# Kernel optimization log

Hardware: AMD Instinct MI355X
Metric: run time of the kernel (lower is better)

## Reference

```python
import jax, jax.numpy as jnp
import numpy as np
import math

B, N, D = 8, 2048, 1024
DK = D // 4
TOP_K = 32
SCALE = math.sqrt(DK)
NEG = -1000000000.0


def setup_inputs() -> dict:
    key = jax.random.key(0)
    k1, k2, k3, k4, k5 = jax.random.split(key, 5)
    lim = 1.0 / math.sqrt(D)
    return {
        "action_states": jax.random.normal(k1, (B, N, D), dtype=jnp.float32),
        "Wq": jax.random.uniform(k2, (D, DK), minval=-lim, maxval=lim, dtype=jnp.float32),
        "bq": jax.random.uniform(k3, (DK,), minval=-lim, maxval=lim, dtype=jnp.float32),
        "Wk": jax.random.uniform(k4, (D, DK), minval=-lim, maxval=lim, dtype=jnp.float32),
        "bk": jax.random.uniform(k5, (DK,), minval=-lim, maxval=lim, dtype=jnp.float32),
    }


def reference(action_states, Wq, bq, Wk, bk):
    # Q, K projections: (B, N, DK)
    Q = jnp.einsum("bnd,dk->bnk", action_states, Wq) + bq
    K = jnp.einsum("bnd,dk->bnk", action_states, Wk) + bk
    # scaled dot-product scores: (B, N, N)
    scores = jnp.einsum("bqk,bmk->bqm", Q, K) / SCALE
    # top-k sparsify per row + scatter mask
    topk_vals, topk_idx = jax.lax.top_k(scores, TOP_K)  # (B, N, K)
    bi = jnp.arange(B)[:, None, None]
    ni = jnp.arange(N)[None, :, None]
    mask = jnp.zeros_like(scores).at[bi, ni, topk_idx].set(1.0)
    scores = scores * mask + (1.0 - mask) * NEG
    return jax.nn.softmax(scores, axis=-1)
```

## Files before the change

### kernel.cpp

```cpp
#include <hip/hip_runtime.h>
#include <cstdint>
#include <cstddef>

#define B_   8
#define N_   2048
#define D_   1024
#define DK_  256
#define M_   (B_ * N_)
#define TOPK 32
#define NDIG 5

typedef unsigned short ushort_t;
typedef float  fvec4 __attribute__((ext_vector_type(4)));
typedef short  bvec8 __attribute__((ext_vector_type(8)));
typedef float  avec4 __attribute__((ext_vector_type(4)));
typedef int    ivec4 __attribute__((ext_vector_type(4)));

__device__ inline ushort_t f32_to_bf16_rn(float f) {
  unsigned u = __float_as_uint(f);
  u += 0x7fffu + ((u >> 16) & 1u);
  return (ushort_t)(u >> 16);
}
__device__ inline float bf16_to_f32(ushort_t u) {
  return __uint_as_float(((unsigned)u) << 16);
}


__global__ __launch_bounds__(256) void split_x_kernel(
    const float* __restrict__ X, signed char* __restrict__ Xdig)
{
  const size_t MK = (size_t)M_ * D_;
  const int total = (int)(MK / 4);
  for (int idx = blockIdx.x * 256 + threadIdx.x; idx < total;
       idx += gridDim.x * 256) {
    const fvec4 x = ((const fvec4*)X)[idx];
    unsigned pack[NDIG] = {0u, 0u, 0u, 0u, 0u};
#pragma unroll
    for (int e = 0; e < 4; e++) {
      float s = x[e] * 0.0625f * 128.f;
#pragma unroll
      for (int d = 0; d < NDIG; d++) {
        const float a = rintf(s);
        s = (s - a) * 128.f;
        pack[d] |= ((unsigned)((int)a & 0xff)) << (e * 8);
      }
    }
#pragma unroll
    for (int d = 0; d < NDIG; d++)
      ((unsigned*)(Xdig + (size_t)d * MK))[idx] = pack[d];
  }
}

__global__ __launch_bounds__(256) void split_w_kernel(
    const float* __restrict__ Wq, const float* __restrict__ Wk,
    signed char* __restrict__ Wdig)
{
  const size_t WK = (size_t)512 * 1024;
  const int cc = blockIdx.x;
  const float* Wp = (cc < 256) ? Wq : Wk;
  const int c = cc & 255;
  const int k0 = threadIdx.x * 4;
  unsigned pack[NDIG] = {0u, 0u, 0u, 0u, 0u};
#pragma unroll
  for (int e = 0; e < 4; e++) {
    float s = Wp[(size_t)(k0 + e) * DK_ + c] * 16.f * 128.f;
#pragma unroll
    for (int d = 0; d < NDIG; d++) {
      const float a = rintf(s);
      s = (s - a) * 128.f;
      pack[d] |= ((unsigned)((int)a & 0xff)) << (e * 8);
    }
  }
#pragma unroll
  for (int d = 0; d < NDIG; d++)
    ((unsigned*)(Wdig + (size_t)d * WK + (size_t)cc * 1024))[threadIdx.x] = pack[d];
}

__global__ __launch_bounds__(512) void ozaki_gemm_kernel(
    const signed char* __restrict__ Xdig, const signed char* __restrict__ Wdig,
    const float* __restrict__ bq, const float* __restrict__ bk,
    double* __restrict__ Qd, double* __restrict__ Kd,
    ushort_t* __restrict__ Qbf, ushort_t* __restrict__ Kbf)
{
  __shared__ __align__(16) char L[61440];
  const int tid  = threadIdx.x;
  const int lane = tid & 63;
  const int w    = tid >> 6;
  const int wm   = (w >> 2) * 32;
  const int wc   = (w & 3) * 32;
  const int m0   = blockIdx.y * 64;
  const int c0   = blockIdx.x * 128;
  const size_t MK = (size_t)M_ * D_;
  const size_t WK = (size_t)512 * 1024;

  ivec4 acc[NDIG][2][2];
#pragma unroll
  for (int s = 0; s < NDIG; s++)
#pragma unroll
    for (int mi = 0; mi < 2; mi++)
#pragma unroll
      for (int nj = 0; nj < 2; nj++) acc[s][mi][nj] = (ivec4)(0);

  for (int k0 = 0; k0 < D_; k0 += 64) {
    for (int c = tid; c < 1280; c += 512) {
      const int d = c >> 8, rem = c & 255, r = rem >> 2, kp = rem & 3;
      const ivec4 raw = *(const ivec4*)(Xdig + (size_t)d * MK +
                         (size_t)(m0 + r) * D_ + k0 + kp * 16);
      *(ivec4*)&L[d * 4096 + r * 64 + ((kp ^ (r & 3)) << 4)] = raw;
    }
    for (int c = tid; c < 2560; c += 512) {
      const int d = c >> 9, rem = c & 511, r = rem >> 2, kp = rem & 3;
      const ivec4 raw = *(const ivec4*)(Wdig + (size_t)d * WK +
                         (size_t)(c0 + r) * 1024 + k0 + kp * 16);
      *(ivec4*)&L[20480 + d * 8192 + r * 64 + ((kp ^ (r & 3)) << 4)] = raw;
    }
    __syncthreads();

    ivec4 afr[2][NDIG];
#pragma unroll
    for (int mi = 0; mi < 2; mi++) {
      const int r = wm + mi * 16 + (lane & 15);
      const int sl = (((lane >> 4) ^ (r & 3)) << 4);
#pragma unroll
      for (int d = 0; d < NDIG; d++)
        afr[mi][d] = *(const ivec4*)&L[d * 4096 + r * 64 + sl];
    }
#pragma unroll
    for (int nj = 0; nj < 2; nj++) {
      const int rc = wc + nj * 16 + (lane & 15);
      const int sl = (((lane >> 4) ^ (rc & 3)) << 4);
#pragma unroll
      for (int jd = 0; jd < NDIG; jd++) {
        const ivec4 bfr = *(const ivec4*)&L[20480 + jd * 8192 + rc * 64 + sl];
#pragma unroll
        for (int id = 0; id + jd < NDIG; id++)
#pragma unroll
          for (int mi = 0; mi < 2; mi++)
            acc[id + jd][mi][nj] = __builtin_amdgcn_mfma_i32_16x16x64_i8(
                afr[mi][id], bfr, acc[id + jd][mi][nj], 0, 0, 0);
      }
    }
    __syncthreads();
  }

  const double SCL[NDIG] = {0x1p-14, 0x1p-21, 0x1p-28, 0x1p-35, 0x1p-42};
#pragma unroll
  for (int nj = 0; nj < 2; nj++) {
    const int c = c0 + wc + nj * 16 + (lane & 15);
    const bool isQ = (c < 256);
    const int cw = isQ ? c : (c - 256);
    const double bias = (double)(isQ ? bq[cw] : bk[cw]);
#pragma unroll
    for (int mi = 0; mi < 2; mi++) {
#pragma unroll
      for (int ri = 0; ri < 4; ri++) {
        const int m = m0 + wm + mi * 16 + (lane >> 4) * 4 + ri;
        double val = bias;
#pragma unroll
        for (int s = 0; s < NDIG; s++)
          val += (double)acc[s][mi][nj][ri] * SCL[s];
        const size_t off = (size_t)m * DK_ + cw;
        if (isQ) { Qd[off] = val; Qbf[off] = f32_to_bf16_rn((float)val); }
        else     { Kd[off] = val; Kbf[off] = f32_to_bf16_rn((float)val); }
      }
    }
  }
}

__global__ __launch_bounds__(256) void proj_kernel(
    const float* __restrict__ X, const float* __restrict__ Wq,
    const float* __restrict__ bq, const float* __restrict__ Wk,
    const float* __restrict__ bk, double* __restrict__ Qd,
    double* __restrict__ Kd, ushort_t* __restrict__ Qbf,
    ushort_t* __restrict__ Kbf)
{
  __shared__ float As[16][132];
  __shared__ float Bs[16][132];
  const int tid = threadIdx.x;
  const int tx = tid & 15;
  const int ty = tid >> 4;
  const int m0 = blockIdx.y * 128;
  const int j0 = blockIdx.x * 128;
  const bool isQ = (j0 < 256);
  const float* Wp = isQ ? Wq : Wk;
  const float* bp = isQ ? bq : bk;
  const int jw = isQ ? j0 : (j0 - 256);

  double acc[8][8];
#pragma unroll
  for (int i = 0; i < 8; i++)
#pragma unroll
    for (int j = 0; j < 8; j++) acc[i][j] = 0.0;

  for (int k0 = 0; k0 < D_; k0 += 16) {
    {
      const int r = tid >> 2, k4 = (tid & 3) * 4;
#pragma unroll
      for (int p = 0; p < 2; p++) {
        const int m = r + 64 * p;
        const fvec4 v = *(const fvec4*)&X[(size_t)(m0 + m) * D_ + k0 + k4];
#pragma unroll
        for (int c = 0; c < 4; c++) As[k4 + c][m] = v[c];
      }
    }
    {
      const int k = tid >> 4, j8 = (tid & 15) * 8;
      const fvec4 v0 = *(const fvec4*)&Wp[(size_t)(k0 + k) * DK_ + jw + j8];
      const fvec4 v1 = *(const fvec4*)&Wp[(size_t)(k0 + k) * DK_ + jw + j8 + 4];
      *(fvec4*)&Bs[k][j8]     = v0;
      *(fvec4*)&Bs[k][j8 + 4] = v1;
    }
    __syncthreads();
#pragma unroll
    for (int kk = 0; kk < 16; kk++) {
      const fvec4 a0 = *(const fvec4*)&As[kk][ty * 8];
      const fvec4 a1 = *(const fvec4*)&As[kk][ty * 8 + 4];
      const fvec4 b0 = *(const fvec4*)&Bs[kk][tx * 8];
      const fvec4 b1 = *(const fvec4*)&Bs[kk][tx * 8 + 4];
      double a[8], b[8];
#pragma unroll
      for (int i = 0; i < 4; i++) {
        a[i] = (double)a0[i]; a[i + 4] = (double)a1[i];
        b[i] = (double)b0[i]; b[i + 4] = (double)b1[i];
      }
#pragma unroll
      for (int i = 0; i < 8; i++)
#pragma unroll
        for (int j = 0; j < 8; j++)
          acc[i][j] = fma(a[i], b[j], acc[i][j]);
    }
    __syncthreads();
  }

#pragma unroll
  for (int i = 0; i < 8; i++) {
    const int m = m0 + ty * 8 + i;
#pragma unroll
    for (int j = 0; j < 8; j++) {
      const int c = jw + tx * 8 + j;
      const double v = acc[i][j] + (double)bp[c];
      const size_t off = (size_t)m * DK_ + c;
      if (isQ) { Qd[off] = v; if (Qbf) Qbf[off] = f32_to_bf16_rn((float)v); }
      else     { Kd[off] = v; if (Kbf) Kbf[off] = f32_to_bf16_rn((float)v); }
    }
  }
}

__global__ __launch_bounds__(256) void score_bf16_kernel(
    const ushort_t* __restrict__ Qb, const ushort_t* __restrict__ Kb,
    float* __restrict__ outf, ushort_t* __restrict__ outbf)
{
  __shared__ ushort_t Asl[128 * 40];
  __shared__ ushort_t Bsl[128 * 40];
  const int tid = threadIdx.x;
  const int b  = blockIdx.z;
  const int q0 = blockIdx.y * 128;
  const int m0 = blockIdx.x * 128;
  const int w = tid >> 6, lane = tid & 63;
  const int wq = (w >> 1) * 64, wm = (w & 1) * 64;
  const int rsel = lane & 15, ksel = (lane >> 4) * 8;

  avec4 acc[4][4];
#pragma unroll
  for (int i = 0; i < 4; i++)
#pragma unroll
    for (int j = 0; j < 4; j++) acc[i][j] = (avec4)(0.f);

  for (int k0 = 0; k0 < DK_; k0 += 32) {
#pragma unroll
    for (int cc = 0; cc < 2; cc++) {
      const int c = tid + cc * 256;
      const int r = c >> 2, part = c & 3;
      const ivec4 va = *(const ivec4*)&Qb[((size_t)b * N_ + q0 + r) * DK_ + k0 + part * 8];
      const ivec4 vb = *(const ivec4*)&Kb[((size_t)b * N_ + m0 + r) * DK_ + k0 + part * 8];
      *(ivec4*)&Asl[r * 40 + part * 8] = va;
      *(ivec4*)&Bsl[r * 40 + part * 8] = vb;
    }
    __syncthreads();
    bvec8 aF[4], bF[4];
#pragma unroll
    for (int mi = 0; mi < 4; mi++)
      aF[mi] = *(const bvec8*)&Asl[(wq + mi * 16 + rsel) * 40 + ksel];
#pragma unroll
    for (int nj = 0; nj < 4; nj++)
      bF[nj] = *(const bvec8*)&Bsl[(wm + nj * 16 + rsel) * 40 + ksel];
#pragma unroll
    for (int mi = 0; mi < 4; mi++)
#pragma unroll
      for (int nj = 0; nj < 4; nj++)
        acc[mi][nj] = __builtin_amdgcn_mfma_f32_16x16x32_bf16(
            aF[mi], bF[nj], acc[mi][nj], 0, 0, 0);
    __syncthreads();
  }

#pragma unroll
  for (int mi = 0; mi < 4; mi++)
#pragma unroll
    for (int nj = 0; nj < 4; nj++)
#pragma unroll
      for (int r = 0; r < 4; r++) {
        const int row = q0 + wq + mi * 16 + (lane >> 4) * 4 + r;
        const int col = m0 + wm + nj * 16 + (lane & 15);
        const size_t off = ((size_t)b * N_ + row) * N_ + col;
        const float v = acc[mi][nj][r] * 0.0625f;
        if (outbf) outbf[off] = f32_to_bf16_rn(v);
        else       outf[off] = v;
      }
}

__global__ __launch_bounds__(256) void score_f64_kernel(
    const double* __restrict__ Qd, const double* __restrict__ Kd,
    float* __restrict__ out)
{
  __shared__ float As[16][68];
  __shared__ float Bs[16][68];
  const int tid = threadIdx.x;
  const int tx = tid & 15, ty = tid >> 4;
  const int b  = blockIdx.z;
  const int q0 = blockIdx.y * 64;
  const int m0 = blockIdx.x * 64;
  const size_t rowbase = (size_t)b * N_;

  float acc[4][4];
#pragma unroll
  for (int i = 0; i < 4; i++)
#pragma unroll
    for (int j = 0; j < 4; j++) acc[i][j] = 0.f;

  for (int k0 = 0; k0 < DK_; k0 += 16) {
    const int mt = tid >> 4, kt = tid & 15;
#pragma unroll
    for (int p = 0; p < 4; p++) {
      const int m = mt + 16 * p;
      As[kt][m] = (float)Qd[(rowbase + q0 + m) * DK_ + k0 + kt];
      Bs[kt][m] = (float)Kd[(rowbase + m0 + m) * DK_ + k0 + kt];
    }
    __syncthreads();
#pragma unroll
    for (int kk = 0; kk < 16; kk++) {
      float a[4], bb[4];
#pragma unroll
      for (int i = 0; i < 4; i++) a[i] = As[kk][ty * 4 + i];
#pragma unroll
      for (int j = 0; j < 4; j++) bb[j] = Bs[kk][tx * 4 + j];
#pragma unroll
      for (int i = 0; i < 4; i++)
#pragma unroll
        for (int j = 0; j < 4; j++)
          acc[i][j] = fmaf(a[i], bb[j], acc[i][j]);
    }
    __syncthreads();
  }

#pragma unroll
  for (int i = 0; i < 4; i++) {
    const size_t r = (size_t)b * N_ + q0 + ty * 4 + i;
#pragma unroll
    for (int j = 0; j < 4; j++)
      out[r * N_ + m0 + tx * 4 + j] = acc[i][j] * 0.0625f;
  }
}

__global__ __launch_bounds__(256) void topk_softmax_kernel(
    float* __restrict__ out, const ushort_t* __restrict__ sbf,
    const float* __restrict__ sf, const double* __restrict__ Qd,
    const double* __restrict__ Kd, float margin)
{
  const int row = blockIdx.x;
  const int b   = row >> 11;
  const int tid = threadIdx.x;
  float* rowp = out + (size_t)row * N_;

  __shared__ float    s[N_];
  __shared__ double   qrow[DK_];
  __shared__ unsigned hist[256];
  __shared__ unsigned sfx[256];
  __shared__ int      cidx[128];
  __shared__ double   cval[128];
  __shared__ int      ncand_s;
  __shared__ unsigned prefix_s;
  __shared__ int      want_s;
  __shared__ double   wmax[4];
  __shared__ float    wsum[4];

  if (sbf) {
    const ivec4 v = *(const ivec4*)&sbf[(size_t)row * N_ + tid * 8];
    const ushort_t* u = (const ushort_t*)&v;
#pragma unroll
    for (int c = 0; c < 8; c++) s[tid * 8 + c] = bf16_to_f32(u[c]);
  } else {
#pragma unroll
    for (int p = 0; p < 2; p++) {
      const fvec4 v = *(const fvec4*)&sf[(size_t)row * N_ + tid * 8 + p * 4];
#pragma unroll
      for (int c = 0; c < 4; c++) s[tid * 8 + p * 4 + c] = v[c];
    }
  }
  qrow[tid] = Qd[(size_t)row * DK_ + tid];
  __syncthreads();

  unsigned prefix = 0;
  int want = TOPK;
  for (int pass = 0; pass < 2; pass++) {
    hist[tid] = 0;
    __syncthreads();
    const int shift_b = 8 - 8 * pass;
    for (int i = tid; i < N_; i += 256) {
      unsigned u = __float_as_uint(s[i]);
      u = (u & 0x80000000u) ? ~u : (u | 0x80000000u);
      const unsigned key = u >> 16;
      const bool ok = (pass == 0) || ((key >> 8) == prefix);
      if (ok) atomicAdd(&hist[(key >> shift_b) & 255u], 1u);
    }
    __syncthreads();
    sfx[tid] = hist[tid];
    __syncthreads();
    for (int st = 1; st < 256; st <<= 1) {
      const unsigned add = (tid + st < 256) ? sfx[tid + st] : 0u;
      __syncthreads();
      sfx[tid] += add;
      __syncthreads();
    }
    const int gt = (int)(sfx[tid] - hist[tid]);
    if (gt < want && (int)sfx[tid] >= want) {
      prefix_s = (prefix << 8) | (unsigned)tid;
      want_s = want - gt;
    }
    __syncthreads();
    prefix = prefix_s;
    want = want_s;
    __syncthreads();
  }
  const unsigned k16 = prefix;
  unsigned ulo;
  if (k16 & 0x8000u) ulo = (k16 << 16) ^ 0x80000000u;
  else               ulo = ~(k16 << 16);
  const float cthr = __uint_as_float(ulo) - margin;

  if (tid == 0) ncand_s = 0;
  __syncthreads();
  for (int i = tid; i < N_; i += 256) {
    if (s[i] >= cthr) {
      const int p = atomicAdd(&ncand_s, 1);
      if (p < 128) cidx[p] = i;
    }
  }
  __syncthreads();
  int nc = ncand_s;
  if (nc > 128) nc = 128;

  const int wid = tid >> 6, lane = tid & 63;
  for (int base = 0; base < nc; base += 4) {
    const int c = base + wid;
    if (c < nc) {
      const double* kp = Kd + ((size_t)b * N_ + cidx[c]) * DK_;
      double a = 0.0;
#pragma unroll
      for (int q = 0; q < 4; q++)
        a = fma(qrow[lane * 4 + q], kp[lane * 4 + q], a);
#pragma unroll
      for (int off = 32; off > 0; off >>= 1) a += __shfl_xor(a, off);
      if (lane == 0) cval[c] = a * 0.0625;
    }
  }
  __syncthreads();

  bool sel = false;
  double v = 0.0;
  int myidx = 0;
  if (tid < nc) {
    v = cval[tid];
    myidx = cidx[tid];
    int rank = 0;
    for (int j = 0; j < nc; j++) {
      const double vj = cval[j];
      rank += (vj > v) || (vj == v && cidx[j] < myidx);
    }
    sel = (rank < TOPK);
  }
  double mv = (tid < nc) ? v : -1.0e300;
#pragma unroll
  for (int off = 32; off > 0; off >>= 1) {
    const double o = __shfl_xor(mv, off);
    mv = o > mv ? o : mv;
  }
  if (lane == 0) wmax[wid] = mv;
  __syncthreads();
  const double vmax = max(max(wmax[0], wmax[1]), max(wmax[2], wmax[3]));
  const float ev = sel ? expf((float)(v - vmax)) : 0.f;
  float es = ev;
#pragma unroll
  for (int off = 32; off > 0; off >>= 1) es += __shfl_xor(es, off);
  if (lane == 0) wsum[wid] = es;
  __syncthreads();
  const float esum = wsum[0] + wsum[1] + wsum[2] + wsum[3];

  for (int i = tid; i < N_; i += 256) s[i] = 0.f;
  __syncthreads();
  if (sel) s[myidx] = ev / esum;
  __syncthreads();
  for (int i = tid; i < N_; i += 256) rowp[i] = s[i];
}

extern "C" void kernel_launch(void* const* d_in, const int* in_sizes, int n_in,
                              void* d_out, int out_size, void* d_ws,
                              size_t ws_size, hipStream_t stream)
{
  const float* X  = (const float*)d_in[0];
  const float* Wq = (const float*)d_in[1];
  const float* bq = (const float*)d_in[2];
  const float* Wk = (const float*)d_in[3];
  const float* bk = (const float*)d_in[4];
  float* out = (float*)d_out;

  const size_t qk = (size_t)M_ * DK_;
  const size_t f64_bytes  = qk * 8 * 2;
  const size_t bf_bytes   = qk * 2 * 2;
  const size_t base       = f64_bytes + bf_bytes;
  const size_t xdig_bytes = (size_t)M_ * D_ * NDIG;
  const size_t wdig_bytes = (size_t)512 * 1024 * NDIG;
  const size_t sbf_bytes  = (size_t)M_ * N_ * 2;
  const size_t oz_total = base + xdig_bytes + wdig_bytes;
  const size_t sc_total = base + sbf_bytes;
  if (ws_size < f64_bytes) return;

  double* Qd = (double*)d_ws;
  double* Kd = Qd + qk;
  ushort_t* Qbf = (ushort_t*)(Kd + qk);
  ushort_t* Kbf = Qbf + qk;
  char* region = (char*)d_ws + base;

  dim3 blk(256);
  if (ws_size >= oz_total) {
    signed char* Xdig = (signed char*)region;
    signed char* Wdig = Xdig + xdig_bytes;
    split_x_kernel<<<2048, blk, 0, stream>>>(X, Xdig);
    split_w_kernel<<<512, blk, 0, stream>>>(Wq, Wk, Wdig);
    ozaki_gemm_kernel<<<dim3(4, 256), dim3(512), 0, stream>>>(
        Xdig, Wdig, bq, bk, Qd, Kd, Qbf, Kbf);
    score_bf16_kernel<<<dim3(N_ / 128, N_ / 128, B_), blk, 0, stream>>>(
        Qbf, Kbf, out, (ushort_t*)region);
    topk_softmax_kernel<<<dim3(M_), blk, 0, stream>>>(
        out, (ushort_t*)region, (const float*)nullptr, Qd, Kd, 1.6e-2f);
    return;
  }

  const bool bfpath = (ws_size >= base);
  const bool scpath = (ws_size >= sc_total);
  proj_kernel<<<dim3(4, 128), blk, 0, stream>>>(
      X, Wq, bq, Wk, bk, Qd, Kd, bfpath ? Qbf : (ushort_t*)nullptr,
      bfpath ? Kbf : (ushort_t*)nullptr);
  if (bfpath) {
    score_bf16_kernel<<<dim3(N_ / 128, N_ / 128, B_), blk, 0, stream>>>(
        Qbf, Kbf, out, scpath ? (ushort_t*)region : (ushort_t*)nullptr);
    if (scpath)
      topk_softmax_kernel<<<dim3(M_), blk, 0, stream>>>(
          out, (ushort_t*)region, (const float*)nullptr, Qd, Kd, 1.6e-2f);
    else
      topk_softmax_kernel<<<dim3(M_), blk, 0, stream>>>(
          out, (const ushort_t*)nullptr, out, Qd, Kd, 8e-3f);
  } else {
    score_f64_kernel<<<dim3(N_ / 64, N_ / 64, B_), blk, 0, stream>>>(Qd, Kd, out);
    topk_softmax_kernel<<<dim3(M_), blk, 0, stream>>>(
        out, (const ushort_t*)nullptr, out, Qd, Kd, 2.5e-4f);
  }
}
```

Before: 486.8 us.

## Replace radix top-k softmax with register binary-search select and sparse scatter

```diff
diff --git a/kernel.cpp b/kernel.cpp
--- a/kernel.cpp
+++ b/kernel.cpp
@@ -24,7 +24,14 @@
 __device__ inline float bf16_to_f32(ushort_t u) {
   return __uint_as_float(((unsigned)u) << 16);
 }
-
+__device__ inline unsigned bf16_key(ushort_t h) {
+  return (h & 0x8000u) ? (unsigned)((~h) & 0xFFFFu) : (unsigned)(h | 0x8000u);
+}
+__device__ inline float key_to_f32(unsigned k) {
+  const ushort_t h = (k & 0x8000u) ? (ushort_t)(k ^ 0x8000u)
+                                   : (ushort_t)((~k) & 0xFFFFu);
+  return bf16_to_f32(h);
+}
 
 __global__ __launch_bounds__(256) void split_x_kernel(
     const float* __restrict__ X, signed char* __restrict__ Xdig)
@@ -361,6 +368,113 @@
   }
 }
 
+__global__ __launch_bounds__(256) void topk_scatter_kernel(
+    float* __restrict__ out, const ushort_t* __restrict__ sbf,
+    const double* __restrict__ Qd, const double* __restrict__ Kd,
+    float margin)
+{
+  const int bid = blockIdx.x;
+  const int row = (bid & 7) * 2048 + (bid >> 3);
+  const int b   = row >> 11;
+  const int tid = threadIdx.x;
+  const int lane = tid & 63, wid = tid >> 6;
+
+  __shared__ double   qrow[DK_];
+  __shared__ int      cidx[128];
+  __shared__ double   cval[128];
+  __shared__ int      cnt_ws[4];
+  __shared__ int      ncand_s;
+  __shared__ double   wmax[4];
+  __shared__ float    wsum[4];
+
+  const ivec4 v = *(const ivec4*)&sbf[(size_t)row * N_ + tid * 8];
+  const ushort_t* u = (const ushort_t*)&v;
+  unsigned kk[8];
+  float    fv[8];
+#pragma unroll
+  for (int e = 0; e < 8; e++) {
+    kk[e] = bf16_key(u[e]);
+    fv[e] = bf16_to_f32(u[e]);
+  }
+  qrow[tid] = Qd[(size_t)row * DK_ + tid];
+  if (tid == 0) ncand_s = 0;
+
+  unsigned lo = 0, hi = 65535;
+#pragma unroll 1
+  for (int it = 0; it < 16; it++) {
+    const unsigned mid = (lo + hi + 1) >> 1;
+    int c = 0;
+#pragma unroll
+    for (int e = 0; e < 8; e++) c += (kk[e] >= mid);
+#pragma unroll
+    for (int off = 32; off > 0; off >>= 1) c += __shfl_xor(c, off);
+    if (lane == 0) cnt_ws[wid] = c;
+    __syncthreads();
+    const int tot = cnt_ws[0] + cnt_ws[1] + cnt_ws[2] + cnt_ws[3];
+    if (tot >= TOPK) lo = mid; else hi = mid - 1;
+    __syncthreads();
+  }
+  const float cthr = key_to_f32(lo) - margin;
+
+#pragma unroll
+  for (int e = 0; e < 8; e++) {
+    if (fv[e] >= cthr) {
+      const int p = atomicAdd(&ncand_s, 1);
+      if (p < 128) cidx[p] = tid * 8 + e;
+    }
+  }
+  __syncthreads();
+  int nc = ncand_s;
+  if (nc > 128) nc = 128;
+
+  for (int base = 0; base < nc; base += 4) {
+    const int c = base + wid;
+    if (c < nc) {
+      const double* kp = Kd + ((size_t)b * N_ + cidx[c]) * DK_;
+      double a = 0.0;
+#pragma unroll
+      for (int q = 0; q < 4; q++)
+        a = fma(qrow[lane * 4 + q], kp[lane * 4 + q], a);
+#pragma unroll
+      for (int off = 32; off > 0; off >>= 1) a += __shfl_xor(a, off);
+      if (lane == 0) cval[c] = a * 0.0625;
+    }
+  }
+  __syncthreads();
+
+  bool sel = false;
+  double vv = 0.0;
+  int myidx = 0;
+  if (tid < nc) {
+    vv = cval[tid];
+    myidx = cidx[tid];
+    int rank = 0;
+    for (int j = 0; j < nc; j++) {
+      const double vj = cval[j];
+      rank += (vj > vv) || (vj == vv && cidx[j] < myidx);
+    }
+    sel = (rank < TOPK);
+  }
+  double mv = (tid < nc) ? vv : -1.0e300;
+#pragma unroll
+  for (int off = 32; off > 0; off >>= 1) {
+    const double o = __shfl_xor(mv, off);
+    mv = o > mv ? o : mv;
+  }
+  if (lane == 0) wmax[wid] = mv;
+  __syncthreads();
+  const double vmax = max(max(wmax[0], wmax[1]), max(wmax[2], wmax[3]));
+  const float ev = sel ? expf((float)(vv - vmax)) : 0.f;
+  float es = ev;
+#pragma unroll
+  for (int off = 32; off > 0; off >>= 1) es += __shfl_xor(es, off);
+  if (lane == 0) wsum[wid] = es;
+  __syncthreads();
+  const float esum = wsum[0] + wsum[1] + wsum[2] + wsum[3];
+
+  if (sel) out[(size_t)row * N_ + myidx] = ev / esum;
+}
+
 __global__ __launch_bounds__(256) void topk_softmax_kernel(
     float* __restrict__ out, const ushort_t* __restrict__ sbf,
     const float* __restrict__ sf, const double* __restrict__ Qd,
@@ -406,9 +520,9 @@
     __syncthreads();
     const int shift_b = 8 - 8 * pass;
     for (int i = tid; i < N_; i += 256) {
-      unsigned u = __float_as_uint(s[i]);
-      u = (u & 0x80000000u) ? ~u : (u | 0x80000000u);
-      const unsigned key = u >> 16;
+      unsigned uu = __float_as_uint(s[i]);
+      uu = (uu & 0x80000000u) ? ~uu : (uu | 0x80000000u);
+      const unsigned key = uu >> 16;
       const bool ok = (pass == 0) || ((key >> 8) == prefix);
       if (ok) atomicAdd(&hist[(key >> shift_b) & 255u], 1u);
     }
@@ -534,14 +648,15 @@
   if (ws_size >= oz_total) {
     signed char* Xdig = (signed char*)region;
     signed char* Wdig = Xdig + xdig_bytes;
+    hipMemsetAsync(out, 0, (size_t)M_ * N_ * sizeof(float), stream);
     split_x_kernel<<<2048, blk, 0, stream>>>(X, Xdig);
     split_w_kernel<<<512, blk, 0, stream>>>(Wq, Wk, Wdig);
     ozaki_gemm_kernel<<<dim3(4, 256), dim3(512), 0, stream>>>(
         Xdig, Wdig, bq, bk, Qd, Kd, Qbf, Kbf);
     score_bf16_kernel<<<dim3(N_ / 128, N_ / 128, B_), blk, 0, stream>>>(
         Qbf, Kbf, out, (ushort_t*)region);
-    topk_softmax_kernel<<<dim3(M_), blk, 0, stream>>>(
-        out, (ushort_t*)region, (const float*)nullptr, Qd, Kd, 1.6e-2f);
+    topk_scatter_kernel<<<dim3(M_), blk, 0, stream>>>(
+        out, (ushort_t*)region, Qd, Kd, 2.5e-2f);
     return;
   }
 
```

Measured after the change: 512.3 us. 5.3% more time.
